# Optimization experiments

Hardware: AMD Instinct MI355X
Metric: run time of the kernel (lower is better)

The kernel has to match this reference:

```python
import jax, jax.numpy as jnp
import numpy as np

LEAK = 0.2

def setup_inputs() -> dict:
    key = jax.random.key(0)
    ks = jax.random.split(key, 8)
    B, D, H1, H2, F = 2048, 3072, 512, 256, 100
    s = lambda fan_in: 1.0 / np.sqrt(fan_in)
    return {
        "x":  jax.random.normal(ks[0], (B, D), dtype=jnp.float32),
        "W1": jax.random.uniform(ks[1], (D, H1), jnp.float32, -s(D), s(D)),
        "b1": jnp.zeros((H1,), jnp.float32),
        "W2": jax.random.uniform(ks[2], (H1, H2), jnp.float32, -s(H1), s(H1)),
        "b2": jnp.zeros((H2,), jnp.float32),
        "T":  jax.random.normal(ks[3], (H2, F), dtype=jnp.float32),
        "Wf": jax.random.uniform(ks[4], (H2 + F, 1), jnp.float32, -s(H2 + F), s(H2 + F)),
        "bf": jnp.zeros((1,), jnp.float32),
    }

def reference(x, W1, b1, W2, b2, T, Wf, bf):
    # MLP stack with LeakyReLU(0.2)
    h = jax.nn.leaky_relu(x @ W1 + b1, LEAK)          # (B,512)
    h = jax.nn.leaky_relu(h @ W2 + b2, LEAK)          # (B,256)
    # Minibatch discrimination: pairwise L1 per feature, exp, sum over batch
    m = h @ T                                          # (B,100)
    d = jnp.abs(m[:, None, :] - m[None, :, :])         # (B,B,100)
    feats = jnp.sum(jnp.exp(-d), axis=1)               # (B,100)
    z = jnp.concatenate([h, feats], axis=1)            # (B,356)
    return z @ Wf + bf                                 # (B,1)
```

## Files before the change

kernel.cpp:

```cpp
#include <hip/hip_runtime.h>
#include <hip/hip_bf16.h>

#define LEAK 0.2f

typedef __attribute__((ext_vector_type(8))) short short8;
typedef __attribute__((ext_vector_type(4))) float f32x4;

__global__ __launch_bounds__(256) void k_prep(const float* __restrict__ x,
                                              __hip_bfloat16* __restrict__ xb,
                                              const float* __restrict__ W1,
                                              __hip_bfloat16* __restrict__ W1t,
                                              const float* __restrict__ W2,
                                              __hip_bfloat16* __restrict__ W2t,
                                              const float* __restrict__ T,
                                              __hip_bfloat16* __restrict__ Tt) {
  int b = blockIdx.x;
  int t = threadIdx.x;
  if (b < 6144) {
    int idx = b * 256 + t;
    float4 v = reinterpret_cast<const float4*>(x)[idx];
    union { ushort4 u; __hip_bfloat16 h[4]; } c;
    c.h[0] = __float2bfloat16(v.x);
    c.h[1] = __float2bfloat16(v.y);
    c.h[2] = __float2bfloat16(v.z);
    c.h[3] = __float2bfloat16(v.w);
    reinterpret_cast<ushort4*>(xb)[idx] = c.u;
    return;
  }
  __shared__ float tile[32][33];
  const float* W;
  __hip_bfloat16* Wt;
  int K, N, kblk, nblk;
  int b2 = b - 6144;
  if (b2 < 1536) {
    W = W1; Wt = W1t; K = 3072; N = 512;
    kblk = b2 % 96; nblk = b2 / 96;
  } else if (b2 < 1664) {
    int b3 = b2 - 1536;
    W = W2; Wt = W2t; K = 512; N = 256;
    kblk = b3 % 16; nblk = b3 / 16;
  } else {
    int b4 = b2 - 1664;
    W = T; Wt = Tt; K = 256; N = 100;
    kblk = b4 % 8; nblk = b4 / 8;
  }
  int k0 = kblk * 32, n0 = nblk * 32;
  int tx = t & 31, ty = t >> 5;
#pragma unroll
  for (int r = 0; r < 4; ++r) {
    int n = n0 + tx;
    tile[ty + r * 8][tx] = (n < N) ? W[(long)(k0 + ty + r * 8) * N + n] : 0.f;
  }
  __syncthreads();
#pragma unroll
  for (int r = 0; r < 4; ++r)
    Wt[(long)(n0 + ty + r * 8) * K + k0 + tx] = __float2bfloat16(tile[tx][ty + r * 8]);
}

template <bool TRANSP>
__global__ __launch_bounds__(256) void k_gemm(const __hip_bfloat16* __restrict__ A,
                                              const __hip_bfloat16* __restrict__ Bt,
                                              float* __restrict__ Cp,
                                              int M, int N, int K, int KSPL, int ldO) {
  __shared__ __align__(16) __hip_bfloat16 As[64][72];
  __shared__ __align__(16) __hip_bfloat16 Bs[64][72];
  int tid = threadIdx.x;
  int lane = tid & 63;
  int wv = tid >> 6;
  int wm = wv & 1, wn = wv >> 1;
  int quad = lane >> 4, l16 = lane & 15;
  long m0 = (long)blockIdx.x * 64, n0 = (long)blockIdx.y * 64;
  int srow = tid >> 2, scol = (tid & 3) * 16;
  int kStart = blockIdx.z * KSPL;
  const __hip_bfloat16* Ag = A + (m0 + srow) * K + kStart + scol;
  const __hip_bfloat16* Bg = Bt + (n0 + srow) * K + kStart + scol;

  int4 ra0 = *reinterpret_cast<const int4*>(Ag);
  int4 ra1 = *reinterpret_cast<const int4*>(Ag + 8);
  int4 rb0 = *reinterpret_cast<const int4*>(Bg);
  int4 rb1 = *reinterpret_cast<const int4*>(Bg + 8);

  f32x4 acc[2][2] = {};
  for (int kb = 0; kb < KSPL; kb += 64) {
    *reinterpret_cast<int4*>(&As[srow][scol]) = ra0;
    *reinterpret_cast<int4*>(&As[srow][scol + 8]) = ra1;
    *reinterpret_cast<int4*>(&Bs[srow][scol]) = rb0;
    *reinterpret_cast<int4*>(&Bs[srow][scol + 8]) = rb1;
    __syncthreads();
    if (kb + 64 < KSPL) {
      ra0 = *reinterpret_cast<const int4*>(Ag + kb + 64);
      ra1 = *reinterpret_cast<const int4*>(Ag + kb + 72);
      rb0 = *reinterpret_cast<const int4*>(Bg + kb + 64);
      rb1 = *reinterpret_cast<const int4*>(Bg + kb + 72);
    }
#pragma unroll
    for (int half = 0; half < 2; ++half) {
      short8 af[2], bfr[2];
#pragma unroll
      for (int t = 0; t < 2; ++t) {
        af[t]  = *reinterpret_cast<const short8*>(&As[wm * 32 + t * 16 + l16][half * 32 + quad * 8]);
        bfr[t] = *reinterpret_cast<const short8*>(&Bs[wn * 32 + t * 16 + l16][half * 32 + quad * 8]);
      }
#pragma unroll
      for (int tm = 0; tm < 2; ++tm)
#pragma unroll
        for (int tn = 0; tn < 2; ++tn)
          acc[tm][tn] =
              __builtin_amdgcn_mfma_f32_16x16x32_bf16(af[tm], bfr[tn], acc[tm][tn], 0, 0, 0);
    }
    __syncthreads();
  }

  float* Cz = Cp + (long)blockIdx.z * M * N;
#pragma unroll
  for (int tm = 0; tm < 2; ++tm)
#pragma unroll
    for (int tn = 0; tn < 2; ++tn)
#pragma unroll
      for (int r = 0; r < 4; ++r) {
        long gm = m0 + wm * 32 + tm * 16 + quad * 4 + r;
        long gn = n0 + wn * 32 + tn * 16 + l16;
        if (TRANSP) Cz[gn * ldO + gm] = acc[tm][tn][r];
        else        Cz[gm * ldO + gn] = acc[tm][tn][r];
      }
}

template <int NZ, bool OUTF>
__global__ __launch_bounds__(256) void k_comb(const float* __restrict__ P,
                                              const float* __restrict__ bias,
                                              float* __restrict__ Of,
                                              __hip_bfloat16* __restrict__ Ob,
                                              int total4, int nmask) {
  int idx = blockIdx.x * 256 + threadIdx.x;
  if (idx >= total4) return;
  float4 v = reinterpret_cast<const float4*>(P)[idx];
#pragma unroll
  for (int z = 1; z < NZ; ++z) {
    float4 a = reinterpret_cast<const float4*>(P + (long)z * total4 * 4)[idx];
    v.x += a.x; v.y += a.y; v.z += a.z; v.w += a.w;
  }
  int col = (idx * 4) & nmask;
  float4 bs = *reinterpret_cast<const float4*>(bias + col);
  v.x += bs.x; v.y += bs.y; v.z += bs.z; v.w += bs.w;
  v.x = v.x > 0.f ? v.x : LEAK * v.x;
  v.y = v.y > 0.f ? v.y : LEAK * v.y;
  v.z = v.z > 0.f ? v.z : LEAK * v.z;
  v.w = v.w > 0.f ? v.w : LEAK * v.w;
  if (OUTF) reinterpret_cast<float4*>(Of)[idx] = v;
  union { ushort4 u; __hip_bfloat16 h[4]; } c;
  c.h[0] = __float2bfloat16(v.x);
  c.h[1] = __float2bfloat16(v.y);
  c.h[2] = __float2bfloat16(v.z);
  c.h[3] = __float2bfloat16(v.w);
  reinterpret_cast<ushort4*>(Ob)[idx] = c.u;
}

__global__ __launch_bounds__(1024) void k_bucketfeats(const float* __restrict__ mTz,
                                                      float* __restrict__ featsT) {
  __shared__ float sP[2048], sN[2048];
  __shared__ float Sp[2048], Sn[2048];
  __shared__ int Smeta[2048];
  __shared__ short sB[2048];
  __shared__ int cnt[256], bstart[256], bcur[256];
  __shared__ float bsP[256], bsN[256], Pbel[256], Nab[256];
  __shared__ float wred[32];
  __shared__ float sMin, sMax;
  int f = blockIdx.x;
  int t = threadIdx.x;
  int lane = t & 63, wv = t >> 6;
  const long FS = 2048L * 128;
  const float* row = mTz + (long)f * 2048;

  float m[2];
  float lmin = 3.4e38f, lmax = -3.4e38f;
#pragma unroll
  for (int r = 0; r < 2; ++r) {
    int e = t + r * 1024;
    float v = row[e] + row[FS + e] + row[2 * FS + e] + row[3 * FS + e];
    m[r] = v;
    lmin = fminf(lmin, v);
    lmax = fmaxf(lmax, v);
  }
#pragma unroll
  for (int d = 32; d; d >>= 1) {
    lmin = fminf(lmin, __shfl_down(lmin, d));
    lmax = fmaxf(lmax, __shfl_down(lmax, d));
  }
  if (lane == 0) { wred[wv] = lmin; wred[16 + wv] = lmax; }
  if (t < 256) cnt[t] = 0;
  __syncthreads();
  if (t == 0) {
    float a = wred[0], b = wred[16];
    for (int i = 1; i < 16; ++i) { a = fminf(a, wred[i]); b = fmaxf(b, wred[16 + i]); }
    sMin = a; sMax = b;
  }
  __syncthreads();
  float mn = sMin, mx = sMax;
  float rge = mx - mn;
  float scale = (rge > 1e-20f) ? 255.0f / rge : 0.f;
  float mid = 0.5f * (mn + mx);
#pragma unroll
  for (int r = 0; r < 2; ++r) {
    int e = t + r * 1024;
    float v = m[r];
    int b = (int)((v - mn) * scale);
    b = b < 255 ? b : 255;
    float arg = fminf(fmaxf(v - mid, -60.f), 60.f);
    sP[e] = __expf(arg);
    sN[e] = __expf(-arg);
    sB[e] = (short)b;
    atomicAdd(&cnt[b], 1);
  }
  __syncthreads();
  if (wv == 0) {
    int b4 = lane * 4;
    int c0 = cnt[b4], c1 = cnt[b4 + 1], c2 = cnt[b4 + 2], c3 = cnt[b4 + 3];
    int tot = c0 + c1 + c2 + c3;
    int inc = tot;
#pragma unroll
    for (int d = 1; d < 64; d <<= 1) {
      int y = __shfl_up(inc, d);
      if (lane >= d) inc += y;
    }
    int run = inc - tot;
    bstart[b4] = run; bcur[b4] = run; run += c0;
    bstart[b4 + 1] = run; bcur[b4 + 1] = run; run += c1;
    bstart[b4 + 2] = run; bcur[b4 + 2] = run; run += c2;
    bstart[b4 + 3] = run; bcur[b4 + 3] = run;
  }
  __syncthreads();
#pragma unroll
  for (int r = 0; r < 2; ++r) {
    int e = t + r * 1024;
    int b = sB[e];
    int slot = atomicAdd(&bcur[b], 1);
    Sp[slot] = sP[e];
    Sn[slot] = sN[e];
    Smeta[slot] = (b << 16) | e;
  }
  __syncthreads();
  if (t < 256) {
    int s0 = bstart[t], s1 = s0 + cnt[t];
    float ap = 0.f, an = 0.f;
    for (int q = s0; q < s1; ++q) { ap += Sp[q]; an += Sn[q]; }
    bsP[t] = ap; bsN[t] = an;
  }
  __syncthreads();
  if (wv == 0) {
    int b4 = lane * 4;
    float p0 = bsP[b4], p1 = bsP[b4 + 1], p2 = bsP[b4 + 2], p3 = bsP[b4 + 3];
    float n0 = bsN[b4], n1 = bsN[b4 + 1], n2 = bsN[b4 + 2], n3 = bsN[b4 + 3];
    float tp = p0 + p1 + p2 + p3, tn = n0 + n1 + n2 + n3;
    float ip = tp, in_ = tn;
#pragma unroll
    for (int d = 1; d < 64; d <<= 1) {
      float yp = __shfl_up(ip, d);
      float yn = __shfl_up(in_, d);
      if (lane >= d) { ip += yp; in_ += yn; }
    }
    float totn = __shfl(in_, 63);
    float runp = ip - tp;
    float runn = in_ - tn;
    Pbel[b4] = runp; Nab[b4] = totn - runn - n0; runp += p0; runn += n0;
    Pbel[b4 + 1] = runp; Nab[b4 + 1] = totn - runn - n1; runp += p1; runn += n1;
    Pbel[b4 + 2] = runp; Nab[b4 + 2] = totn - runn - n2; runp += p2; runn += n2;
    Pbel[b4 + 3] = runp; Nab[b4 + 3] = totn - runn - n3;
  }
  __syncthreads();
#pragma unroll
  for (int r = 0; r < 2; ++r) {
    int s = t + r * 1024;
    int meta = Smeta[s];
    int b = meta >> 16;
    int idx = meta & 0xFFFF;
    float p = Sp[s], n = Sn[s];
    float acc = n * Pbel[b] + p * Nab[b];
    int q0 = bstart[b], q1 = q0 + cnt[b];
    for (int q = q0; q < q1; ++q) acc += fminf(p * Sn[q], n * Sp[q]);
    featsT[(long)f * 2048 + idx] = acc;
  }
}

__global__ __launch_bounds__(256) void k_final(const float* __restrict__ h2f,
                                               const float* __restrict__ featsT,
                                               const float* __restrict__ Wf,
                                               const float* __restrict__ bfp,
                                               float* __restrict__ out) {
  int wv = threadIdx.x >> 6, lane = threadIdx.x & 63;
  long i = (long)blockIdx.x * 4 + wv;
  const float* hrow = h2f + i * 256;
  float s = 0.f;
#pragma unroll
  for (int c = lane; c < 256; c += 64) s += hrow[c] * Wf[c];
  for (int f = lane; f < 100; f += 64) s += featsT[(long)f * 2048 + i] * Wf[256 + f];
#pragma unroll
  for (int off = 32; off; off >>= 1) s += __shfl_down(s, off);
  if (lane == 0) out[i] = s + bfp[0];
}

extern "C" void kernel_launch(void* const* d_in, const int* in_sizes, int n_in,
                              void* d_out, int out_size, void* d_ws, size_t ws_size,
                              hipStream_t stream) {
  const float* x  = (const float*)d_in[0];
  const float* W1 = (const float*)d_in[1];
  const float* b1 = (const float*)d_in[2];
  const float* W2 = (const float*)d_in[3];
  const float* b2 = (const float*)d_in[4];
  const float* T  = (const float*)d_in[5];
  const float* Wf = (const float*)d_in[6];
  const float* bf = (const float*)d_in[7];
  float* out = (float*)d_out;

  char* w = (char*)d_ws;
  auto alloc = [&](size_t b) { char* p = w; w += (b + 255) & ~(size_t)255; return p; };
  __hip_bfloat16* xb  = (__hip_bfloat16*)alloc(2048L * 3072 * 2);
  __hip_bfloat16* W1t = (__hip_bfloat16*)alloc(512L * 3072 * 2);
  __hip_bfloat16* W2t = (__hip_bfloat16*)alloc(256L * 512 * 2);
  __hip_bfloat16* Tt  = (__hip_bfloat16*)alloc(128L * 256 * 2);
  __hip_bfloat16* h1b = (__hip_bfloat16*)alloc(2048L * 512 * 2);
  float*          h2f = (float*)alloc(2048L * 256 * 4);
  __hip_bfloat16* h2b = (__hip_bfloat16*)alloc(2048L * 256 * 2);
  float*          feT = (float*)alloc(100L * 2048 * 4);
  float*          P1  = (float*)alloc(3L * 2048 * 512 * 4);
  float*          P2  = (float*)alloc(2L * 2048 * 256 * 4);
  float*          P3  = (float*)alloc(4L * 2048 * 128 * 4);

  k_prep<<<7840, 256, 0, stream>>>(x, xb, W1, W1t, W2, W2t, T, Tt);
  k_gemm<false><<<dim3(32, 8, 3), 256, 0, stream>>>(xb, W1t, P1, 2048, 512, 3072, 1024, 512);
  k_comb<3, false><<<1024, 256, 0, stream>>>(P1, b1, nullptr, h1b, 262144, 511);
  k_gemm<false><<<dim3(32, 4, 2), 256, 0, stream>>>(h1b, W2t, P2, 2048, 256, 512, 256, 256);
  k_comb<2, true><<<512, 256, 0, stream>>>(P2, b2, h2f, h2b, 131072, 255);
  k_gemm<true><<<dim3(32, 2, 4), 256, 0, stream>>>(h2b, Tt, P3, 2048, 128, 256, 64, 2048);
  k_bucketfeats<<<100, 1024, 0, stream>>>(P3, feT);
  k_final<<<512, 256, 0, stream>>>(h2f, feT, Wf, bf, out);
}
```

Before: 129.3 us.

## Use direct global-to-LDS loads in GEMM and fuse final projection into prior kernels

The GEMM now stages tiles with global_load_lds straight into double-buffered, XOR-swizzled LDS instead of going through registers, overlapping the next tile's load with the current MFMA work. The final linear layer is split up: the h2 half of the dot product is computed in a new row-wise combine kernel, and the feats half is accumulated with atomicAdd inside the bucket-features kernel. This removes the k_final launch and the h2f and featsT round trips through memory. In exchange it adds about 200K float atomics to the output and makes the summation order nondeterministic.

```diff
diff --git a/kernel.cpp b/kernel.cpp
--- a/kernel.cpp
+++ b/kernel.cpp
@@ -5,6 +5,13 @@
 
 typedef __attribute__((ext_vector_type(8))) short short8;
 typedef __attribute__((ext_vector_type(4))) float f32x4;
+
+typedef __attribute__((address_space(3))) unsigned int lds_u32;
+typedef const __attribute__((address_space(1))) unsigned int glb_u32;
+
+__device__ __forceinline__ void gload16(const void* g, void* l) {
+  __builtin_amdgcn_global_load_lds((glb_u32*)g, (lds_u32*)l, 16, 0, 0);
+}
 
 __global__ __launch_bounds__(256) void k_prep(const float* __restrict__ x,
                                               __hip_bfloat16* __restrict__ xb,
@@ -62,44 +69,48 @@
                                               const __hip_bfloat16* __restrict__ Bt,
                                               float* __restrict__ Cp,
                                               int M, int N, int K, int KSPL, int ldO) {
-  __shared__ __align__(16) __hip_bfloat16 As[64][72];
-  __shared__ __align__(16) __hip_bfloat16 Bs[64][72];
+  __shared__ __align__(16) char sm[2][2][8192];
   int tid = threadIdx.x;
   int lane = tid & 63;
   int wv = tid >> 6;
   int wm = wv & 1, wn = wv >> 1;
   int quad = lane >> 4, l16 = lane & 15;
+  int sx = (l16 & 7) << 4;
   long m0 = (long)blockIdx.x * 64, n0 = (long)blockIdx.y * 64;
-  int srow = tid >> 2, scol = (tid & 3) * 16;
   int kStart = blockIdx.z * KSPL;
-  const __hip_bfloat16* Ag = A + (m0 + srow) * K + kStart + scol;
-  const __hip_bfloat16* Bg = Bt + (n0 + srow) * K + kStart + scol;
-
-  int4 ra0 = *reinterpret_cast<const int4*>(Ag);
-  int4 ra1 = *reinterpret_cast<const int4*>(Ag + 8);
-  int4 rb0 = *reinterpret_cast<const int4*>(Bg);
-  int4 rb1 = *reinterpret_cast<const int4*>(Bg + 8);
+
+  int srow = wv * 16 + (lane >> 3);
+  int scolb = ((lane & 7) ^ (lane >> 3)) << 4;
+  const char* Ag = (const char*)(A + (m0 + srow) * K + kStart) + scolb;
+  const char* Bg = (const char*)(Bt + (n0 + srow) * K + kStart) + scolb;
+  long rowB = (long)K * 2 * 8;
+
+  auto STAGE = [&](int buf, int kb2) {
+    char* base = &sm[buf][0][0] + wv * 2048;
+    gload16(Ag + kb2, base);
+    gload16(Ag + kb2 + rowB, base + 1024);
+    gload16(Bg + kb2, base + 8192);
+    gload16(Bg + kb2 + rowB, base + 8192 + 1024);
+  };
 
   f32x4 acc[2][2] = {};
-  for (int kb = 0; kb < KSPL; kb += 64) {
-    *reinterpret_cast<int4*>(&As[srow][scol]) = ra0;
-    *reinterpret_cast<int4*>(&As[srow][scol + 8]) = ra1;
-    *reinterpret_cast<int4*>(&Bs[srow][scol]) = rb0;
-    *reinterpret_cast<int4*>(&Bs[srow][scol + 8]) = rb1;
-    __syncthreads();
-    if (kb + 64 < KSPL) {
-      ra0 = *reinterpret_cast<const int4*>(Ag + kb + 64);
-      ra1 = *reinterpret_cast<const int4*>(Ag + kb + 72);
-      rb0 = *reinterpret_cast<const int4*>(Bg + kb + 64);
-      rb1 = *reinterpret_cast<const int4*>(Bg + kb + 72);
-    }
+  int nt = KSPL >> 6;
+  STAGE(0, 0);
+  asm volatile("s_waitcnt vmcnt(0)" ::: "memory");
+  __builtin_amdgcn_s_barrier();
+  int cur = 0;
+  for (int t = 0; t < nt; ++t) {
+    if (t + 1 < nt) STAGE(cur ^ 1, (t + 1) << 7);
+    const char* smA = &sm[cur][0][0];
+    const char* smB = &sm[cur][1][0];
 #pragma unroll
     for (int half = 0; half < 2; ++half) {
       short8 af[2], bfr[2];
-#pragma unroll
-      for (int t = 0; t < 2; ++t) {
-        af[t]  = *reinterpret_cast<const short8*>(&As[wm * 32 + t * 16 + l16][half * 32 + quad * 8]);
-        bfr[t] = *reinterpret_cast<const short8*>(&Bs[wn * 32 + t * 16 + l16][half * 32 + quad * 8]);
+      int cb = (half * 64 + quad * 16) ^ sx;
+#pragma unroll
+      for (int tt = 0; tt < 2; ++tt) {
+        af[tt]  = *reinterpret_cast<const short8*>(smA + (wm * 32 + tt * 16 + l16) * 128 + cb);
+        bfr[tt] = *reinterpret_cast<const short8*>(smB + (wn * 32 + tt * 16 + l16) * 128 + cb);
       }
 #pragma unroll
       for (int tm = 0; tm < 2; ++tm)
@@ -108,7 +119,9 @@
           acc[tm][tn] =
               __builtin_amdgcn_mfma_f32_16x16x32_bf16(af[tm], bfr[tn], acc[tm][tn], 0, 0, 0);
     }
-    __syncthreads();
+    asm volatile("s_waitcnt vmcnt(0)" ::: "memory");
+    __builtin_amdgcn_s_barrier();
+    cur ^= 1;
   }
 
   float* Cz = Cp + (long)blockIdx.z * M * N;
@@ -125,10 +138,9 @@
       }
 }
 
-template <int NZ, bool OUTF>
+template <int NZ>
 __global__ __launch_bounds__(256) void k_comb(const float* __restrict__ P,
                                               const float* __restrict__ bias,
-                                              float* __restrict__ Of,
                                               __hip_bfloat16* __restrict__ Ob,
                                               int total4, int nmask) {
   int idx = blockIdx.x * 256 + threadIdx.x;
@@ -146,7 +158,6 @@
   v.y = v.y > 0.f ? v.y : LEAK * v.y;
   v.z = v.z > 0.f ? v.z : LEAK * v.z;
   v.w = v.w > 0.f ? v.w : LEAK * v.w;
-  if (OUTF) reinterpret_cast<float4*>(Of)[idx] = v;
   union { ushort4 u; __hip_bfloat16 h[4]; } c;
   c.h[0] = __float2bfloat16(v.x);
   c.h[1] = __float2bfloat16(v.y);
@@ -155,8 +166,40 @@
   reinterpret_cast<ushort4*>(Ob)[idx] = c.u;
 }
 
+__global__ __launch_bounds__(256) void k_comb2row(const float* __restrict__ P,
+                                                  const float* __restrict__ bias,
+                                                  const float* __restrict__ Wf,
+                                                  const float* __restrict__ bfp,
+                                                  __hip_bfloat16* __restrict__ h2b,
+                                                  float* __restrict__ out) {
+  int wv = threadIdx.x >> 6, lane = threadIdx.x & 63;
+  long i = (long)blockIdx.x * 4 + wv;
+  long off = i * 256 + lane * 4;
+  float4 v = *reinterpret_cast<const float4*>(P + off);
+  float4 a = *reinterpret_cast<const float4*>(P + 2048L * 256 + off);
+  v.x += a.x; v.y += a.y; v.z += a.z; v.w += a.w;
+  float4 bs = *reinterpret_cast<const float4*>(bias + lane * 4);
+  v.x += bs.x; v.y += bs.y; v.z += bs.z; v.w += bs.w;
+  v.x = v.x > 0.f ? v.x : LEAK * v.x;
+  v.y = v.y > 0.f ? v.y : LEAK * v.y;
+  v.z = v.z > 0.f ? v.z : LEAK * v.z;
+  v.w = v.w > 0.f ? v.w : LEAK * v.w;
+  union { ushort4 u; __hip_bfloat16 h[4]; } c;
+  c.h[0] = __float2bfloat16(v.x);
+  c.h[1] = __float2bfloat16(v.y);
+  c.h[2] = __float2bfloat16(v.z);
+  c.h[3] = __float2bfloat16(v.w);
+  reinterpret_cast<ushort4*>(h2b)[i * 64 + lane] = c.u;
+  float4 wfv = *reinterpret_cast<const float4*>(Wf + lane * 4);
+  float s = v.x * wfv.x + v.y * wfv.y + v.z * wfv.z + v.w * wfv.w;
+#pragma unroll
+  for (int d = 32; d; d >>= 1) s += __shfl_down(s, d);
+  if (lane == 0) out[i] = s + bfp[0];
+}
+
 __global__ __launch_bounds__(1024) void k_bucketfeats(const float* __restrict__ mTz,
-                                                      float* __restrict__ featsT) {
+                                                      const float* __restrict__ Wf,
+                                                      float* __restrict__ out) {
   __shared__ float sP[2048], sN[2048];
   __shared__ float Sp[2048], Sn[2048];
   __shared__ int Smeta[2048];
@@ -170,6 +213,7 @@
   int lane = t & 63, wv = t >> 6;
   const long FS = 2048L * 128;
   const float* row = mTz + (long)f * 2048;
+  float wf = Wf[256 + f];
 
   float m[2];
   float lmin = 3.4e38f, lmax = -3.4e38f;
@@ -277,25 +321,8 @@
     float acc = n * Pbel[b] + p * Nab[b];
     int q0 = bstart[b], q1 = q0 + cnt[b];
     for (int q = q0; q < q1; ++q) acc += fminf(p * Sn[q], n * Sp[q]);
-    featsT[(long)f * 2048 + idx] = acc;
-  }
-}
-
-__global__ __launch_bounds__(256) void k_final(const float* __restrict__ h2f,
-                                               const float* __restrict__ featsT,
-                                               const float* __restrict__ Wf,
-                                               const float* __restrict__ bfp,
-                                               float* __restrict__ out) {
-  int wv = threadIdx.x >> 6, lane = threadIdx.x & 63;
-  long i = (long)blockIdx.x * 4 + wv;
-  const float* hrow = h2f + i * 256;
-  float s = 0.f;
-#pragma unroll
-  for (int c = lane; c < 256; c += 64) s += hrow[c] * Wf[c];
-  for (int f = lane; f < 100; f += 64) s += featsT[(long)f * 2048 + i] * Wf[256 + f];
-#pragma unroll
-  for (int off = 32; off; off >>= 1) s += __shfl_down(s, off);
-  if (lane == 0) out[i] = s + bfp[0];
+    atomicAdd(&out[idx], acc * wf);
+  }
 }
 
 extern "C" void kernel_launch(void* const* d_in, const int* in_sizes, int n_in,
@@ -318,19 +345,16 @@
   __hip_bfloat16* W2t = (__hip_bfloat16*)alloc(256L * 512 * 2);
   __hip_bfloat16* Tt  = (__hip_bfloat16*)alloc(128L * 256 * 2);
   __hip_bfloat16* h1b = (__hip_bfloat16*)alloc(2048L * 512 * 2);
-  float*          h2f = (float*)alloc(2048L * 256 * 4);
   __hip_bfloat16* h2b = (__hip_bfloat16*)alloc(2048L * 256 * 2);
-  float*          feT = (float*)alloc(100L * 2048 * 4);
   float*          P1  = (float*)alloc(3L * 2048 * 512 * 4);
   float*          P2  = (float*)alloc(2L * 2048 * 256 * 4);
   float*          P3  = (float*)alloc(4L * 2048 * 128 * 4);
 
   k_prep<<<7840, 256, 0, stream>>>(x, xb, W1, W1t, W2, W2t, T, Tt);
   k_gemm<false><<<dim3(32, 8, 3), 256, 0, stream>>>(xb, W1t, P1, 2048, 512, 3072, 1024, 512);
-  k_comb<3, false><<<1024, 256, 0, stream>>>(P1, b1, nullptr, h1b, 262144, 511);
+  k_comb<3><<<1024, 256, 0, stream>>>(P1, b1, h1b, 262144, 511);
   k_gemm<false><<<dim3(32, 4, 2), 256, 0, stream>>>(h1b, W2t, P2, 2048, 256, 512, 256, 256);
-  k_comb<2, true><<<512, 256, 0, stream>>>(P2, b2, h2f, h2b, 131072, 255);
+  k_comb2row<<<512, 256, 0, stream>>>(P2, b2, Wf, bf, h2b, out);
   k_gemm<true><<<dim3(32, 2, 4), 256, 0, stream>>>(h2b, Tt, P3, 2048, 128, 256, 64, 2048);
-  k_bucketfeats<<<100, 1024, 0, stream>>>(P3, feT);
-  k_final<<<512, 256, 0, stream>>>(h2f, feT, Wf, bf, out);
-}
+  k_bucketfeats<<<100, 1024, 0, stream>>>(P3, Wf, out);
+}
```

After: 150.8 us. 16.6% more time.

## Use 128x64 tile GEMM for layer 1 and fuse h2 dot into combine

Applied to the files above, without the earlier changes.

Adds a dedicated first-layer GEMM with 128x64 tiles, a 4-way K split, and register prefetch of the next K block, raising MFMA work per shared-memory load. The second-layer combine kernel now also computes the h2·Wf partial dot product and writes it to the output. This removes the fp32 h2 buffer and its reread in the final kernel. The final kernel only adds the features contribution, at the cost of one more partial buffer to reduce for layer 1.

```diff
diff --git a/kernel.cpp b/kernel.cpp
--- a/kernel.cpp
+++ b/kernel.cpp
@@ -57,6 +57,76 @@
     Wt[(long)(n0 + ty + r * 8) * K + k0 + tx] = __float2bfloat16(tile[tx][ty + r * 8]);
 }
 
+__global__ __launch_bounds__(256) void k_gemm1(const __hip_bfloat16* __restrict__ A,
+                                               const __hip_bfloat16* __restrict__ Bt,
+                                               float* __restrict__ Cp,
+                                               int K, int KSPL) {
+  __shared__ __align__(16) __hip_bfloat16 As[128][72];
+  __shared__ __align__(16) __hip_bfloat16 Bs[64][72];
+  int tid = threadIdx.x;
+  int lane = tid & 63;
+  int wv = tid >> 6;
+  int wm = wv & 1, wn = wv >> 1;
+  int quad = lane >> 4, l16 = lane & 15;
+  long m0 = (long)blockIdx.x * 128, n0 = (long)blockIdx.y * 64;
+  int srow = tid >> 3, scol = (tid & 7) * 8;
+  int kStart = blockIdx.z * KSPL;
+  const __hip_bfloat16* Ag = A + (m0 + srow) * K + kStart + scol;
+  const __hip_bfloat16* Bg = Bt + (n0 + srow) * K + kStart + scol;
+
+  int4 ra[4], rb[2];
+#pragma unroll
+  for (int p = 0; p < 4; ++p) ra[p] = *reinterpret_cast<const int4*>(Ag + (long)p * 32 * K);
+#pragma unroll
+  for (int p = 0; p < 2; ++p) rb[p] = *reinterpret_cast<const int4*>(Bg + (long)p * 32 * K);
+
+  f32x4 acc[4][2] = {};
+  for (int kb = 0; kb < KSPL; kb += 64) {
+#pragma unroll
+    for (int p = 0; p < 4; ++p) *reinterpret_cast<int4*>(&As[srow + p * 32][scol]) = ra[p];
+#pragma unroll
+    for (int p = 0; p < 2; ++p) *reinterpret_cast<int4*>(&Bs[srow + p * 32][scol]) = rb[p];
+    __syncthreads();
+    if (kb + 64 < KSPL) {
+#pragma unroll
+      for (int p = 0; p < 4; ++p)
+        ra[p] = *reinterpret_cast<const int4*>(Ag + (long)p * 32 * K + kb + 64);
+#pragma unroll
+      for (int p = 0; p < 2; ++p)
+        rb[p] = *reinterpret_cast<const int4*>(Bg + (long)p * 32 * K + kb + 64);
+    }
+#pragma unroll
+    for (int half = 0; half < 2; ++half) {
+      short8 af[4], bfr[2];
+#pragma unroll
+      for (int tm = 0; tm < 4; ++tm)
+        af[tm] = *reinterpret_cast<const short8*>(&As[wm * 64 + tm * 16 + l16][half * 32 + quad * 8]);
+#pragma unroll
+      for (int tn = 0; tn < 2; ++tn)
+        bfr[tn] = *reinterpret_cast<const short8*>(&Bs[wn * 32 + tn * 16 + l16][half * 32 + quad * 8]);
+#pragma unroll
+      for (int tm = 0; tm < 4; ++tm)
+#pragma unroll
+        for (int tn = 0; tn < 2; ++tn)
+          acc[tm][tn] =
+              __builtin_amdgcn_mfma_f32_16x16x32_bf16(af[tm], bfr[tn], acc[tm][tn], 0, 0, 0);
+    }
+    __syncthreads();
+  }
+
+  float* Cz = Cp + (long)blockIdx.z * 2048 * 512;
+#pragma unroll
+  for (int tm = 0; tm < 4; ++tm)
+#pragma unroll
+    for (int tn = 0; tn < 2; ++tn)
+#pragma unroll
+      for (int r = 0; r < 4; ++r) {
+        long gm = m0 + wm * 64 + tm * 16 + quad * 4 + r;
+        long gn = n0 + wn * 32 + tn * 16 + l16;
+        Cz[gm * 512 + gn] = acc[tm][tn][r];
+      }
+}
+
 template <bool TRANSP>
 __global__ __launch_bounds__(256) void k_gemm(const __hip_bfloat16* __restrict__ A,
                                               const __hip_bfloat16* __restrict__ Bt,
@@ -125,10 +195,9 @@
       }
 }
 
-template <int NZ, bool OUTF>
+template <int NZ>
 __global__ __launch_bounds__(256) void k_comb(const float* __restrict__ P,
                                               const float* __restrict__ bias,
-                                              float* __restrict__ Of,
                                               __hip_bfloat16* __restrict__ Ob,
                                               int total4, int nmask) {
   int idx = blockIdx.x * 256 + threadIdx.x;
@@ -146,13 +215,43 @@
   v.y = v.y > 0.f ? v.y : LEAK * v.y;
   v.z = v.z > 0.f ? v.z : LEAK * v.z;
   v.w = v.w > 0.f ? v.w : LEAK * v.w;
-  if (OUTF) reinterpret_cast<float4*>(Of)[idx] = v;
   union { ushort4 u; __hip_bfloat16 h[4]; } c;
   c.h[0] = __float2bfloat16(v.x);
   c.h[1] = __float2bfloat16(v.y);
   c.h[2] = __float2bfloat16(v.z);
   c.h[3] = __float2bfloat16(v.w);
   reinterpret_cast<ushort4*>(Ob)[idx] = c.u;
+}
+
+__global__ __launch_bounds__(256) void k_comb2row(const float* __restrict__ P,
+                                                  const float* __restrict__ bias,
+                                                  const float* __restrict__ Wf,
+                                                  const float* __restrict__ bfp,
+                                                  __hip_bfloat16* __restrict__ h2b,
+                                                  float* __restrict__ out) {
+  int wv = threadIdx.x >> 6, lane = threadIdx.x & 63;
+  long i = (long)blockIdx.x * 4 + wv;
+  long off = i * 256 + lane * 4;
+  float4 v = *reinterpret_cast<const float4*>(P + off);
+  float4 a = *reinterpret_cast<const float4*>(P + 2048L * 256 + off);
+  v.x += a.x; v.y += a.y; v.z += a.z; v.w += a.w;
+  float4 bs = *reinterpret_cast<const float4*>(bias + lane * 4);
+  v.x += bs.x; v.y += bs.y; v.z += bs.z; v.w += bs.w;
+  v.x = v.x > 0.f ? v.x : LEAK * v.x;
+  v.y = v.y > 0.f ? v.y : LEAK * v.y;
+  v.z = v.z > 0.f ? v.z : LEAK * v.z;
+  v.w = v.w > 0.f ? v.w : LEAK * v.w;
+  union { ushort4 u; __hip_bfloat16 h[4]; } c;
+  c.h[0] = __float2bfloat16(v.x);
+  c.h[1] = __float2bfloat16(v.y);
+  c.h[2] = __float2bfloat16(v.z);
+  c.h[3] = __float2bfloat16(v.w);
+  reinterpret_cast<ushort4*>(h2b)[i * 64 + lane] = c.u;
+  float4 wfv = *reinterpret_cast<const float4*>(Wf + lane * 4);
+  float s = v.x * wfv.x + v.y * wfv.y + v.z * wfv.z + v.w * wfv.w;
+#pragma unroll
+  for (int d = 32; d; d >>= 1) s += __shfl_down(s, d);
+  if (lane == 0) out[i] = s + bfp[0];
 }
 
 __global__ __launch_bounds__(1024) void k_bucketfeats(const float* __restrict__ mTz,
@@ -281,21 +380,14 @@
   }
 }
 
-__global__ __launch_bounds__(256) void k_final(const float* __restrict__ h2f,
-                                               const float* __restrict__ featsT,
-                                               const float* __restrict__ Wf,
-                                               const float* __restrict__ bfp,
-                                               float* __restrict__ out) {
-  int wv = threadIdx.x >> 6, lane = threadIdx.x & 63;
-  long i = (long)blockIdx.x * 4 + wv;
-  const float* hrow = h2f + i * 256;
+__global__ __launch_bounds__(256) void k_final2(const float* __restrict__ featsT,
+                                                const float* __restrict__ Wf,
+                                                float* __restrict__ out) {
+  int i = blockIdx.x * 256 + threadIdx.x;
   float s = 0.f;
-#pragma unroll
-  for (int c = lane; c < 256; c += 64) s += hrow[c] * Wf[c];
-  for (int f = lane; f < 100; f += 64) s += featsT[(long)f * 2048 + i] * Wf[256 + f];
-#pragma unroll
-  for (int off = 32; off; off >>= 1) s += __shfl_down(s, off);
-  if (lane == 0) out[i] = s + bfp[0];
+#pragma unroll 4
+  for (int f = 0; f < 100; ++f) s += featsT[(long)f * 2048 + i] * Wf[256 + f];
+  out[i] += s;
 }
 
 extern "C" void kernel_launch(void* const* d_in, const int* in_sizes, int n_in,
@@ -318,19 +410,18 @@
   __hip_bfloat16* W2t = (__hip_bfloat16*)alloc(256L * 512 * 2);
   __hip_bfloat16* Tt  = (__hip_bfloat16*)alloc(128L * 256 * 2);
   __hip_bfloat16* h1b = (__hip_bfloat16*)alloc(2048L * 512 * 2);
-  float*          h2f = (float*)alloc(2048L * 256 * 4);
   __hip_bfloat16* h2b = (__hip_bfloat16*)alloc(2048L * 256 * 2);
   float*          feT = (float*)alloc(100L * 2048 * 4);
-  float*          P1  = (float*)alloc(3L * 2048 * 512 * 4);
+  float*          P1  = (float*)alloc(4L * 2048 * 512 * 4);
   float*          P2  = (float*)alloc(2L * 2048 * 256 * 4);
   float*          P3  = (float*)alloc(4L * 2048 * 128 * 4);
 
   k_prep<<<7840, 256, 0, stream>>>(x, xb, W1, W1t, W2, W2t, T, Tt);
-  k_gemm<false><<<dim3(32, 8, 3), 256, 0, stream>>>(xb, W1t, P1, 2048, 512, 3072, 1024, 512);
-  k_comb<3, false><<<1024, 256, 0, stream>>>(P1, b1, nullptr, h1b, 262144, 511);
+  k_gemm1<<<dim3(16, 8, 4), 256, 0, stream>>>(xb, W1t, P1, 3072, 768);
+  k_comb<4><<<1024, 256, 0, stream>>>(P1, b1, h1b, 262144, 511);
   k_gemm<false><<<dim3(32, 4, 2), 256, 0, stream>>>(h1b, W2t, P2, 2048, 256, 512, 256, 256);
-  k_comb<2, true><<<512, 256, 0, stream>>>(P2, b2, h2f, h2b, 131072, 255);
+  k_comb2row<<<512, 256, 0, stream>>>(P2, b2, Wf, bf, h2b, out);
   k_gemm<true><<<dim3(32, 2, 4), 256, 0, stream>>>(h2b, Tt, P3, 2048, 128, 256, 64, 2048);
   k_bucketfeats<<<100, 1024, 0, stream>>>(P3, feT);
-  k_final<<<512, 256, 0, stream>>>(h2f, feT, Wf, bf, out);
-}
+  k_final2<<<8, 256, 0, stream>>>(feT, Wf, out);
+}
```

New measurement: 167.2 us. +29.3%, slower.
